# Kernel tuning notes

Hardware: AMD Instinct MI355X
Metric: run time of the kernel (lower is better)

## Reference

```python
import jax, jax.numpy as jnp
import numpy as np

LATENT = 128
N_NODES = 50000
N_EDGES = 800000
LN_EPS = 1e-5


def _glorot(key, fan_in, fan_out):
    lim = np.sqrt(6.0 / (fan_in + fan_out)).astype(np.float32)
    return jax.random.uniform(key, (fan_in, fan_out), jnp.float32, -lim, lim)


def setup_inputs() -> dict:
    key = jax.random.key(0)
    ks = jax.random.split(key, 10)
    node_latents = jax.random.normal(ks[0], (1, N_NODES, LATENT), jnp.float32)
    mesh_edge_latents = jax.random.normal(ks[1], (1, N_EDGES, LATENT), jnp.float32)
    senders = jax.random.randint(ks[2], (N_EDGES,), 0, N_NODES, jnp.int32)
    receivers = jax.random.randint(ks[3], (N_EDGES,), 0, N_NODES, jnp.int32)
    # mesh_edge_net: Linear(3L, L), ReLU, Linear(L, L), ReLU, LayerNorm(L)
    me_w1 = _glorot(ks[4], 3 * LATENT, LATENT)
    me_b1 = jnp.zeros((LATENT,), jnp.float32)
    me_w2 = _glorot(ks[5], LATENT, LATENT)
    me_b2 = jnp.zeros((LATENT,), jnp.float32)
    me_g = jnp.ones((LATENT,), jnp.float32)
    me_beta = jnp.zeros((LATENT,), jnp.float32)
    # node_feature_net: Linear(2L, L), ReLU, Linear(L, L), ReLU, LayerNorm(L)
    nf_w1 = _glorot(ks[6], 2 * LATENT, LATENT)
    nf_b1 = jnp.zeros((LATENT,), jnp.float32)
    nf_w2 = _glorot(ks[7], LATENT, LATENT)
    nf_b2 = jnp.zeros((LATENT,), jnp.float32)
    nf_g = jnp.ones((LATENT,), jnp.float32)
    nf_beta = jnp.zeros((LATENT,), jnp.float32)
    return dict(node_latents=node_latents, mesh_edge_latents=mesh_edge_latents,
                senders=senders, receivers=receivers,
                me_w1=me_w1, me_b1=me_b1, me_w2=me_w2, me_b2=me_b2, me_g=me_g, me_beta=me_beta,
                nf_w1=nf_w1, nf_b1=nf_b1, nf_w2=nf_w2, nf_b2=nf_b2, nf_g=nf_g, nf_beta=nf_beta)


def _mlp_ln(x, w1, b1, w2, b2, g, beta):
    h = jax.nn.relu(x @ w1 + b1)
    h = jax.nn.relu(h @ w2 + b2)
    mu = jnp.mean(h, axis=-1, keepdims=True)
    var = jnp.var(h, axis=-1, keepdims=True)
    return (h - mu) * jax.lax.rsqrt(var + LN_EPS) * g + beta


def reference(node_latents, mesh_edge_latents, senders, receivers,
              me_w1, me_b1, me_w2, me_b2, me_g, me_beta,
              nf_w1, nf_b1, nf_w2, nf_b2, nf_g, nf_beta):
    # gather sender/receiver node features: [B, E, L]
    edge_in = jnp.concatenate([node_latents[:, senders, :],
                               node_latents[:, receivers, :],
                               mesh_edge_latents], axis=-1)
    new_edges = _mlp_ln(edge_in, me_w1, me_b1, me_w2, me_b2, me_g, me_beta)
    # scatter_add messages to receiver nodes along dim=1
    aggr = jax.vmap(lambda e: jax.ops.segment_sum(e, receivers, num_segments=N_NODES))(new_edges)
    node_in = jnp.concatenate([node_latents, aggr], axis=-1)
    new_nodes = _mlp_ln(node_in, nf_w1, nf_b1, nf_w2, nf_b2, nf_g, nf_beta)
    new_nodes = new_nodes + node_latents  # residual
    new_edges = new_edges + mesh_edge_latents  # residual
    return new_nodes, new_edges
```

## Files before the change

kernel.cpp:

```cpp
#include <hip/hip_runtime.h>
#include <stdint.h>

typedef unsigned short u16;
typedef __bf16 bf16x8 __attribute__((ext_vector_type(8)));
typedef float f32x4 __attribute__((ext_vector_type(4)));

#define N_NODES 50000
#define N_EDGES 800000
#define LN_EPS 1e-5f

__device__ __forceinline__ uint4 pack8(const float* __restrict__ p) {
    const float4 f0 = ((const float4*)p)[0];
    const float4 f1 = ((const float4*)p)[1];
    union { __bf16 b[8]; uint4 q; } t;
    t.b[0] = (__bf16)f0.x; t.b[1] = (__bf16)f0.y; t.b[2] = (__bf16)f0.z; t.b[3] = (__bf16)f0.w;
    t.b[4] = (__bf16)f1.x; t.b[5] = (__bf16)f1.y; t.b[6] = (__bf16)f1.z; t.b[7] = (__bf16)f1.w;
    return t.q;
}

__global__ void pack_weights(const float* __restrict__ w1e, const float* __restrict__ w2e,
                             const float* __restrict__ w1n, const float* __restrict__ w2n,
                             uint4* __restrict__ out)
{
    const int t = blockIdx.x * 256 + threadIdx.x;
    const float* W; int idx;
    if (t < 6144)       { W = w1e; idx = t; }
    else if (t < 8192)  { W = w2e; idx = t - 6144; }
    else if (t < 12288) { W = w1n; idx = t - 8192; }
    else                { W = w2n; idx = t - 12288; }
    const int lane = idx & 63;
    const int col16 = (idx >> 6) & 7;
    const int kb = idx >> 9;
    const int row0 = kb * 32 + (lane >> 4) * 8;
    const int col = col16 * 16 + (lane & 15);
    union { __bf16 b[8]; uint4 q; } v;
#pragma unroll
    for (int j = 0; j < 8; ++j) v.b[j] = (__bf16)W[(size_t)(row0 + j) * 128 + col];
    out[t] = v.q;
}

__global__ void hist_kernel(const int* __restrict__ receivers, int* __restrict__ cnt) {
    const int e = blockIdx.x * 256 + threadIdx.x;
    if (e < N_EDGES) atomicAdd(&cnt[receivers[e]], 1);
}

__global__ void scan_kernel(const int* __restrict__ cnt, int* __restrict__ cursor) {
    __shared__ int sums[1024];
    const int t = threadIdx.x;
    const int CH = 49;
    const int base = t * CH;
    int s = 0;
#pragma unroll 1
    for (int i = 0; i < CH; ++i) { const int idx = base + i; if (idx < N_NODES) s += cnt[idx]; }
    sums[t] = s;
    __syncthreads();
    for (int off = 1; off < 1024; off <<= 1) {
        const int v = (t >= off) ? sums[t - off] : 0;
        __syncthreads();
        sums[t] += v;
        __syncthreads();
    }
    int run = sums[t] - s;
#pragma unroll 1
    for (int i = 0; i < CH; ++i) {
        const int idx = base + i;
        if (idx < N_NODES) { cursor[idx] = run; run += cnt[idx]; }
    }
}

__global__ void scatter_kernel(const int* __restrict__ receivers, int* __restrict__ cursor,
                               int* __restrict__ sorted_eid) {
    const int e = blockIdx.x * 256 + threadIdx.x;
    if (e < N_EDGES) {
        const int pos = atomicAdd(&cursor[receivers[e]], 1);
        sorted_eid[pos] = e;
    }
}

template<int SORTED>
__global__ __launch_bounds__(256, 3)
void edge_mlp_kernel(const float* __restrict__ node, const float* __restrict__ elat,
                     const int* __restrict__ senders, const int* __restrict__ receivers,
                     const int* __restrict__ sorted_eid,
                     const float* __restrict__ b1, const float* __restrict__ b2,
                     const float* __restrict__ gam, const float* __restrict__ bet,
                     const uint4* __restrict__ w1p, const uint4* __restrict__ w2p,
                     float* __restrict__ eout, float* __restrict__ aggr)
{
    __shared__ __align__(16) u16 x_lds[3 * 64 * 128];
    __shared__ int rcv_s[64];
    __shared__ int eid_s[64];
    __shared__ float2 part[256];
    __shared__ float muv[64], rsv[64];

    float* lnf = (float*)x_lds;

    const int tid = threadIdx.x;
    const int w = tid >> 6;
    const int lane = tid & 63;
    const int cl = lane & 15;
    const int q = lane >> 4;
    const int n_base = w * 32;

    float b1v[2], b2v[2], gv[2], bv[2];
#pragma unroll
    for (int n = 0; n < 2; ++n) {
        const int c = n_base + n * 16 + cl;
        b1v[n] = b1[c]; b2v[n] = b2[c];
        gv[n]  = gam[c]; bv[n] = bet[c];
    }

    for (int tile = blockIdx.x; tile < N_EDGES / 64; tile += gridDim.x) {
        const int base = tile * 64;

        {
            const int ch = tid & 15;
            const int r0 = tid >> 4;
#pragma unroll
            for (int gp = 0; gp < 4; ++gp) {
                const int row = gp * 16 + r0;
                const int rx = row & 7;
                const int eid = SORTED ? sorted_eid[base + row] : (base + row);
                const int sn = senders[eid];
                const int rc = receivers[eid];
                if (ch == 0) { rcv_s[row] = rc; eid_s[row] = eid; }
                uint4* dst = (uint4*)x_lds + row * 16;
                dst[ch ^ rx]          = pack8(node + (size_t)sn * 128 + ch * 8);
                dst[1024 + (ch ^ rx)] = pack8(node + (size_t)rc * 128 + ch * 8);
                dst[2048 + (ch ^ rx)] = pack8(elat + (size_t)eid * 128 + ch * 8);
            }
        }
        __syncthreads();

        f32x4 acc[4][2];
#pragma unroll
        for (int m = 0; m < 4; ++m)
#pragma unroll
            for (int n = 0; n < 2; ++n)
#pragma unroll
                for (int r = 0; r < 4; ++r) acc[m][n][r] = 0.f;

        uint4 wreg[14][2];
#pragma unroll
        for (int kb = 0; kb < 2; ++kb)
#pragma unroll
            for (int n = 0; n < 2; ++n)
                wreg[kb][n] = w1p[(kb * 8 + w * 2 + n) * 64 + lane];

#pragma unroll
        for (int kb = 0; kb < 12; ++kb) {
            if (kb + 2 < 12) {
#pragma unroll
                for (int n = 0; n < 2; ++n)
                    wreg[kb + 2][n] = w1p[((kb + 2) * 8 + w * 2 + n) * 64 + lane];
            }
            const int p = kb >> 2, k2 = kb & 3;
            bf16x8 a[4];
#pragma unroll
            for (int m = 0; m < 4; ++m) {
                const int row = m * 16 + cl;
                a[m] = __builtin_bit_cast(bf16x8,
                    ((const uint4*)x_lds)[p * 1024 + row * 16 + ((k2 * 4 + q) ^ (row & 7))]);
            }
#pragma unroll
            for (int m = 0; m < 4; ++m)
#pragma unroll
                for (int n = 0; n < 2; ++n)
                    acc[m][n] = __builtin_amdgcn_mfma_f32_16x16x32_bf16(
                        a[m], __builtin_bit_cast(bf16x8, wreg[kb][n]), acc[m][n], 0, 0, 0);
        }

        uint4 w2reg[4][2];
#pragma unroll
        for (int kb = 0; kb < 4; ++kb)
#pragma unroll
            for (int n = 0; n < 2; ++n)
                w2reg[kb][n] = w2p[(kb * 8 + w * 2 + n) * 64 + lane];

        __syncthreads();

        {
            __bf16* hb = (__bf16*)x_lds;
#pragma unroll
            for (int m = 0; m < 4; ++m)
#pragma unroll
                for (int n = 0; n < 2; ++n)
#pragma unroll
                    for (int r = 0; r < 4; ++r) {
                        const int row = m * 16 + q * 4 + r;
                        const int col = n_base + n * 16 + cl;
                        hb[row * 128 + (((col >> 3) ^ (row & 7)) << 3) + (col & 7)] =
                            (__bf16)fmaxf(acc[m][n][r] + b1v[n], 0.f);
                    }
        }
        __syncthreads();

#pragma unroll
        for (int m = 0; m < 4; ++m)
#pragma unroll
            for (int n = 0; n < 2; ++n)
#pragma unroll
                for (int r = 0; r < 4; ++r) acc[m][n][r] = 0.f;
#pragma unroll
        for (int kb = 0; kb < 4; ++kb) {
            bf16x8 a[4];
#pragma unroll
            for (int m = 0; m < 4; ++m) {
                const int row = m * 16 + cl;
                a[m] = __builtin_bit_cast(bf16x8,
                    ((const uint4*)x_lds)[row * 16 + ((kb * 4 + q) ^ (row & 7))]);
            }
#pragma unroll
            for (int m = 0; m < 4; ++m)
#pragma unroll
                for (int n = 0; n < 2; ++n)
                    acc[m][n] = __builtin_amdgcn_mfma_f32_16x16x32_bf16(
                        a[m], __builtin_bit_cast(bf16x8, w2reg[kb][n]), acc[m][n], 0, 0, 0);
        }

#pragma unroll
        for (int m = 0; m < 4; ++m)
#pragma unroll
            for (int n = 0; n < 2; ++n)
#pragma unroll
                for (int r = 0; r < 4; ++r)
                    acc[m][n][r] = fmaxf(acc[m][n][r] + b2v[n], 0.f);

#pragma unroll
        for (int m = 0; m < 4; ++m)
#pragma unroll
            for (int r = 0; r < 4; ++r) {
                float s  = acc[m][0][r] + acc[m][1][r];
                float ss = acc[m][0][r] * acc[m][0][r] + acc[m][1][r] * acc[m][1][r];
#pragma unroll
                for (int off = 1; off < 16; off <<= 1) {
                    s  += __shfl_xor(s, off, 64);
                    ss += __shfl_xor(ss, off, 64);
                }
                if (cl == 0) part[w * 64 + m * 16 + q * 4 + r] = make_float2(s, ss);
            }
        __syncthreads();
        if (tid < 64) {
            float s = 0.f, ss = 0.f;
#pragma unroll
            for (int ww = 0; ww < 4; ++ww) { const float2 pp = part[ww * 64 + tid]; s += pp.x; ss += pp.y; }
            const float mu = s * (1.f / 128.f);
            const float var = ss * (1.f / 128.f) - mu * mu;
            muv[tid] = mu;
            rsv[tid] = rsqrtf(var + LN_EPS);
        }
        __syncthreads();

#pragma unroll
        for (int m = 0; m < 4; ++m)
#pragma unroll
            for (int r = 0; r < 4; ++r) {
                const int row = m * 16 + q * 4 + r;
                const float mu = muv[row];
                const float rs = rsv[row];
                float* orow = eout + (size_t)eid_s[row] * 128;
#pragma unroll
                for (int n = 0; n < 2; ++n) {
                    const int col = n_base + n * 16 + cl;
                    const float ln = (acc[m][n][r] - mu) * rs * gv[n] + bv[n];
                    lnf[row * 128 + col] = ln;
                    const float e = (float)((__bf16*)x_lds)[16384 + row * 128 + (((col >> 3) ^ (row & 7)) << 3) + (col & 7)];
                    orow[col] = ln + e;
                }
            }
        __syncthreads();

        {
            const int c = tid & 127;
            const int h = tid >> 7;
            const int rstart = h * 32, rend = rstart + 32;
            float sacc = 0.f; int flushed = 0;
#pragma unroll 1
            for (int r = rstart; r < rend; ++r) {
                sacc += lnf[r * 128 + c];
                const int rc = rcv_s[r];
                const bool last = (r == 63);
                const bool bnd = last || (rc != rcv_s[r + 1]);
                if (bnd) {
                    float* dst = &aggr[(size_t)rc * 128 + c];
                    if (SORTED && !last && flushed) *dst = sacc;
                    else atomicAdd(dst, sacc);
                    sacc = 0.f; flushed = 1;
                }
            }
            if (sacc != 0.f)
                atomicAdd(&aggr[(size_t)rcv_s[rend - 1] * 128 + c], sacc);
        }
        __syncthreads();
    }
}

__global__ __launch_bounds__(256, 4)
void node_mlp_kernel(const float* __restrict__ node, const float* __restrict__ aggr,
                     const float* __restrict__ b1, const float* __restrict__ b2,
                     const float* __restrict__ gam, const float* __restrict__ bet,
                     const uint4* __restrict__ w1p, const uint4* __restrict__ w2p,
                     float* __restrict__ nout)
{
    __shared__ __align__(16) u16 x_lds[2 * 64 * 128];
    __shared__ float2 part[256];
    __shared__ float muv[64], rsv[64];

    const int tid = threadIdx.x;
    const int w = tid >> 6;
    const int lane = tid & 63;
    const int cl = lane & 15;
    const int q = lane >> 4;
    const int n_base = w * 32;

    float b1v[2], b2v[2], gv[2], bv[2];
#pragma unroll
    for (int n = 0; n < 2; ++n) {
        const int c = n_base + n * 16 + cl;
        b1v[n] = b1[c]; b2v[n] = b2[c];
        gv[n]  = gam[c]; bv[n] = bet[c];
    }

    const int ntiles = (N_NODES + 63) / 64;
    for (int tile = blockIdx.x; tile < ntiles; tile += gridDim.x) {
        const int base = tile * 64;

        {
            const int ch = tid & 15;
            const int r0 = tid >> 4;
#pragma unroll
            for (int gp = 0; gp < 4; ++gp) {
                const int row = gp * 16 + r0;
                const int rx = row & 7;
                int gn = base + row;
                if (gn >= N_NODES) gn = N_NODES - 1;
                uint4* dst = (uint4*)x_lds + row * 16;
                dst[ch ^ rx]          = pack8(node + (size_t)gn * 128 + ch * 8);
                dst[1024 + (ch ^ rx)] = pack8(aggr + (size_t)gn * 128 + ch * 8);
            }
        }
        __syncthreads();

        f32x4 acc[4][2];
#pragma unroll
        for (int m = 0; m < 4; ++m)
#pragma unroll
            for (int n = 0; n < 2; ++n)
#pragma unroll
                for (int r = 0; r < 4; ++r) acc[m][n][r] = 0.f;

        uint4 wreg[10][2];
#pragma unroll
        for (int kb = 0; kb < 2; ++kb)
#pragma unroll
            for (int n = 0; n < 2; ++n)
                wreg[kb][n] = w1p[(kb * 8 + w * 2 + n) * 64 + lane];

#pragma unroll
        for (int kb = 0; kb < 8; ++kb) {
            if (kb + 2 < 8) {
#pragma unroll
                for (int n = 0; n < 2; ++n)
                    wreg[kb + 2][n] = w1p[((kb + 2) * 8 + w * 2 + n) * 64 + lane];
            }
            const int p = kb >> 2, k2 = kb & 3;
            bf16x8 a[4];
#pragma unroll
            for (int m = 0; m < 4; ++m) {
                const int row = m * 16 + cl;
                a[m] = __builtin_bit_cast(bf16x8,
                    ((const uint4*)x_lds)[p * 1024 + row * 16 + ((k2 * 4 + q) ^ (row & 7))]);
            }
#pragma unroll
            for (int m = 0; m < 4; ++m)
#pragma unroll
                for (int n = 0; n < 2; ++n)
                    acc[m][n] = __builtin_amdgcn_mfma_f32_16x16x32_bf16(
                        a[m], __builtin_bit_cast(bf16x8, wreg[kb][n]), acc[m][n], 0, 0, 0);
        }

        uint4 w2reg[4][2];
#pragma unroll
        for (int kb = 0; kb < 4; ++kb)
#pragma unroll
            for (int n = 0; n < 2; ++n)
                w2reg[kb][n] = w2p[(kb * 8 + w * 2 + n) * 64 + lane];

        __syncthreads();

        {
            __bf16* hb = (__bf16*)(x_lds + 8192);
#pragma unroll
            for (int m = 0; m < 4; ++m)
#pragma unroll
                for (int n = 0; n < 2; ++n)
#pragma unroll
                    for (int r = 0; r < 4; ++r) {
                        const int row = m * 16 + q * 4 + r;
                        const int col = n_base + n * 16 + cl;
                        hb[row * 128 + (((col >> 3) ^ (row & 7)) << 3) + (col & 7)] =
                            (__bf16)fmaxf(acc[m][n][r] + b1v[n], 0.f);
                    }
        }
        __syncthreads();

#pragma unroll
        for (int m = 0; m < 4; ++m)
#pragma unroll
            for (int n = 0; n < 2; ++n)
#pragma unroll
                for (int r = 0; r < 4; ++r) acc[m][n][r] = 0.f;
#pragma unroll
        for (int kb = 0; kb < 4; ++kb) {
            bf16x8 a[4];
#pragma unroll
            for (int m = 0; m < 4; ++m) {
                const int row = m * 16 + cl;
                a[m] = __builtin_bit_cast(bf16x8,
                    ((const uint4*)x_lds)[1024 + row * 16 + ((kb * 4 + q) ^ (row & 7))]);
            }
#pragma unroll
            for (int m = 0; m < 4; ++m)
#pragma unroll
                for (int n = 0; n < 2; ++n)
                    acc[m][n] = __builtin_amdgcn_mfma_f32_16x16x32_bf16(
                        a[m], __builtin_bit_cast(bf16x8, w2reg[kb][n]), acc[m][n], 0, 0, 0);
        }
#pragma unroll
        for (int m = 0; m < 4; ++m)
#pragma unroll
            for (int n = 0; n < 2; ++n)
#pragma unroll
                for (int r = 0; r < 4; ++r)
                    acc[m][n][r] = fmaxf(acc[m][n][r] + b2v[n], 0.f);

#pragma unroll
        for (int m = 0; m < 4; ++m)
#pragma unroll
            for (int r = 0; r < 4; ++r) {
                float s  = acc[m][0][r] + acc[m][1][r];
                float ss = acc[m][0][r] * acc[m][0][r] + acc[m][1][r] * acc[m][1][r];
#pragma unroll
                for (int off = 1; off < 16; off <<= 1) {
                    s  += __shfl_xor(s, off, 64);
                    ss += __shfl_xor(ss, off, 64);
                }
                if (cl == 0) part[w * 64 + m * 16 + q * 4 + r] = make_float2(s, ss);
            }
        __syncthreads();
        if (tid < 64) {
            float s = 0.f, ss = 0.f;
#pragma unroll
            for (int ww = 0; ww < 4; ++ww) { const float2 pp = part[ww * 64 + tid]; s += pp.x; ss += pp.y; }
            const float mu = s * (1.f / 128.f);
            const float var = ss * (1.f / 128.f) - mu * mu;
            muv[tid] = mu;
            rsv[tid] = rsqrtf(var + LN_EPS);
        }
        __syncthreads();

#pragma unroll
        for (int m = 0; m < 4; ++m)
#pragma unroll
            for (int r = 0; r < 4; ++r) {
                const int row = m * 16 + q * 4 + r;
                if (base + row < N_NODES) {
                    const float mu = muv[row];
                    const float rs = rsv[row];
                    float* orow = nout + (size_t)(base + row) * 128;
#pragma unroll
                    for (int n = 0; n < 2; ++n) {
                        const int col = n_base + n * 16 + cl;
                        const float ln = (acc[m][n][r] - mu) * rs * gv[n] + bv[n];
                        const float e = (float)((__bf16*)x_lds)[row * 128 + (((col >> 3) ^ (row & 7)) << 3) + (col & 7)];
                        orow[col] = ln + e;
                    }
                }
            }
        __syncthreads();
    }
}

extern "C" void kernel_launch(void* const* d_in, const int* in_sizes, int n_in,
                              void* d_out, int out_size, void* d_ws, size_t ws_size,
                              hipStream_t stream) {
    (void)in_sizes; (void)n_in; (void)out_size;
    const float* node = (const float*)d_in[0];
    const float* elat = (const float*)d_in[1];
    const int* senders = (const int*)d_in[2];
    const int* receivers = (const int*)d_in[3];
    const float* me_w1 = (const float*)d_in[4];
    const float* me_b1 = (const float*)d_in[5];
    const float* me_w2 = (const float*)d_in[6];
    const float* me_b2 = (const float*)d_in[7];
    const float* me_g  = (const float*)d_in[8];
    const float* me_be = (const float*)d_in[9];
    const float* nf_w1 = (const float*)d_in[10];
    const float* nf_b1 = (const float*)d_in[11];
    const float* nf_w2 = (const float*)d_in[12];
    const float* nf_b2 = (const float*)d_in[13];
    const float* nf_g  = (const float*)d_in[14];
    const float* nf_be = (const float*)d_in[15];

    float* out_nodes = (float*)d_out;
    float* out_edges = out_nodes + (size_t)N_NODES * 128;

    char* ws = (char*)d_ws;
    const size_t off_aggr   = 0;
    const size_t off_wpack  = off_aggr  + (size_t)N_NODES * 128 * sizeof(float);
    const size_t off_cnt    = off_wpack + 14336 * sizeof(uint4);
    const size_t off_cursor = off_cnt   + (size_t)N_NODES * sizeof(int);
    const size_t off_sorted = off_cursor+ (size_t)N_NODES * sizeof(int);
    const size_t need_full  = off_sorted+ (size_t)N_EDGES * sizeof(int);
    const size_t need_min   = off_cnt;
    if (ws_size < need_min) return;

    float* aggr   = (float*)(ws + off_aggr);
    uint4* wpack  = (uint4*)(ws + off_wpack);
    int*   cnt    = (int*)(ws + off_cnt);
    int*   cursor = (int*)(ws + off_cursor);
    int*   sorted = (int*)(ws + off_sorted);
    const bool use_sort = (ws_size >= need_full);

    hipMemsetAsync(aggr, 0, (size_t)N_NODES * 128 * sizeof(float), stream);
    pack_weights<<<56, 256, 0, stream>>>(me_w1, me_w2, nf_w1, nf_w2, wpack);

    if (use_sort) {
        hipMemsetAsync(cnt, 0, (size_t)N_NODES * sizeof(int), stream);
        hist_kernel<<<(N_EDGES + 255) / 256, 256, 0, stream>>>(receivers, cnt);
        scan_kernel<<<1, 1024, 0, stream>>>(cnt, cursor);
        scatter_kernel<<<(N_EDGES + 255) / 256, 256, 0, stream>>>(receivers, cursor, sorted);
        edge_mlp_kernel<1><<<768, 256, 0, stream>>>(node, elat, senders, receivers, sorted,
                                                    me_b1, me_b2, me_g, me_be,
                                                    wpack, wpack + 6144,
                                                    out_edges, aggr);
    } else {
        edge_mlp_kernel<0><<<768, 256, 0, stream>>>(node, elat, senders, receivers, nullptr,
                                                    me_b1, me_b2, me_g, me_be,
                                                    wpack, wpack + 6144,
                                                    out_edges, aggr);
    }
    node_mlp_kernel<<<782, 256, 0, stream>>>(node, aggr,
                                             nf_b1, nf_b2, nf_g, nf_be,
                                             wpack + 8192, wpack + 12288,
                                             out_nodes);
}
```

Measured before the change: 1.162 ms.

## Pre-convert nodes to bf16, pre-permute edge latents, parallelize scan, chunk tiles

Node latents are converted to bf16 once, and edge latents are permuted into receiver-sorted bf16 order before the edge MLP. The gathers then copy bf16 rows directly instead of converting fp32 on every load. The single-block scan is replaced by a three-kernel parallel scan. The scatter also emits sorted sender and receiver arrays so the edge kernel avoids indirect index lookups, and each block now processes a contiguous, XCD-interleaved range of tiles. The trade-off is an extra full pass over the edge latents in permute_elat, plus reuse of the output buffer as scratch.

```diff
diff --git a/kernel.cpp b/kernel.cpp
--- a/kernel.cpp
+++ b/kernel.cpp
@@ -7,6 +7,7 @@
 
 #define N_NODES 50000
 #define N_EDGES 800000
+#define NTILES  (N_EDGES / 64)
 #define LN_EPS 1e-5f
 
 __device__ __forceinline__ uint4 pack8(const float* __restrict__ p) {
@@ -39,49 +40,82 @@
     out[t] = v.q;
 }
 
+__global__ void convert_node(const float* __restrict__ node, uint4* __restrict__ node_bf) {
+    const int idx = blockIdx.x * 256 + threadIdx.x;
+    node_bf[idx] = pack8(node + (size_t)(idx >> 4) * 128 + (idx & 15) * 8);
+}
+
 __global__ void hist_kernel(const int* __restrict__ receivers, int* __restrict__ cnt) {
     const int e = blockIdx.x * 256 + threadIdx.x;
     if (e < N_EDGES) atomicAdd(&cnt[receivers[e]], 1);
 }
 
-__global__ void scan_kernel(const int* __restrict__ cnt, int* __restrict__ cursor) {
-    __shared__ int sums[1024];
+#define SCAN_NB 196
+__global__ void scan1(const int* __restrict__ cnt, int* __restrict__ bsum) {
+    __shared__ int wsum[4];
+    const int i = blockIdx.x * 256 + threadIdx.x;
+    int v = (i < N_NODES) ? cnt[i] : 0;
+#pragma unroll
+    for (int off = 1; off < 64; off <<= 1) v += __shfl_xor(v, off, 64);
+    if ((threadIdx.x & 63) == 0) wsum[threadIdx.x >> 6] = v;
+    __syncthreads();
+    if (threadIdx.x == 0) bsum[blockIdx.x] = wsum[0] + wsum[1] + wsum[2] + wsum[3];
+}
+__global__ void scan2(const int* __restrict__ bsum, int* __restrict__ boff) {
+    __shared__ int s[256];
     const int t = threadIdx.x;
-    const int CH = 49;
-    const int base = t * CH;
-    int s = 0;
-#pragma unroll 1
-    for (int i = 0; i < CH; ++i) { const int idx = base + i; if (idx < N_NODES) s += cnt[idx]; }
-    sums[t] = s;
-    __syncthreads();
-    for (int off = 1; off < 1024; off <<= 1) {
-        const int v = (t >= off) ? sums[t - off] : 0;
-        __syncthreads();
-        sums[t] += v;
-        __syncthreads();
-    }
-    int run = sums[t] - s;
-#pragma unroll 1
-    for (int i = 0; i < CH; ++i) {
-        const int idx = base + i;
-        if (idx < N_NODES) { cursor[idx] = run; run += cnt[idx]; }
-    }
-}
-
-__global__ void scatter_kernel(const int* __restrict__ receivers, int* __restrict__ cursor,
-                               int* __restrict__ sorted_eid) {
+    const int v = (t < SCAN_NB) ? bsum[t] : 0;
+    s[t] = v; __syncthreads();
+    for (int off = 1; off < 256; off <<= 1) {
+        const int u = (t >= off) ? s[t - off] : 0;
+        __syncthreads(); s[t] += u; __syncthreads();
+    }
+    if (t < SCAN_NB) boff[t] = s[t] - v;
+}
+__global__ void scan3(const int* __restrict__ cnt, const int* __restrict__ boff,
+                      int* __restrict__ cursor) {
+    __shared__ int s[256];
+    const int i = blockIdx.x * 256 + threadIdx.x;
+    const int t = threadIdx.x;
+    const int v = (i < N_NODES) ? cnt[i] : 0;
+    s[t] = v; __syncthreads();
+    for (int off = 1; off < 256; off <<= 1) {
+        const int u = (t >= off) ? s[t - off] : 0;
+        __syncthreads(); s[t] += u; __syncthreads();
+    }
+    if (i < N_NODES) cursor[i] = boff[blockIdx.x] + s[t] - v;
+}
+
+__global__ void scatter_kernel(const int* __restrict__ senders, const int* __restrict__ receivers,
+                               int* __restrict__ cursor,
+                               int* __restrict__ sorted_eid, int* __restrict__ pos_of,
+                               int* __restrict__ snd_sorted, int* __restrict__ rcv_sorted) {
     const int e = blockIdx.x * 256 + threadIdx.x;
     if (e < N_EDGES) {
-        const int pos = atomicAdd(&cursor[receivers[e]], 1);
+        const int rc = receivers[e];
+        const int pos = atomicAdd(&cursor[rc], 1);
         sorted_eid[pos] = e;
-    }
+        pos_of[e] = pos;
+        snd_sorted[pos] = senders[e];
+        rcv_sorted[pos] = rc;
+    }
+}
+
+__global__ void permute_elat(const float* __restrict__ elat, const int* __restrict__ pos_of,
+                             uint4* __restrict__ elat_s) {
+    const int idx = blockIdx.x * 256 + threadIdx.x;
+    const int e = idx >> 4, ch = idx & 15;
+    const int p = pos_of[e];
+    elat_s[(size_t)p * 16 + ch] = pack8(elat + (size_t)e * 128 + ch * 8);
 }
 
 template<int SORTED>
 __global__ __launch_bounds__(256, 3)
-void edge_mlp_kernel(const float* __restrict__ node, const float* __restrict__ elat,
+void edge_mlp_kernel(const u16* __restrict__ node_bf, const float* __restrict__ elat,
+                     const u16* __restrict__ elat_s,
                      const int* __restrict__ senders, const int* __restrict__ receivers,
                      const int* __restrict__ sorted_eid,
+                     const int* __restrict__ snd_sorted, const int* __restrict__ rcv_sorted,
                      const float* __restrict__ b1, const float* __restrict__ b2,
                      const float* __restrict__ gam, const float* __restrict__ bet,
                      const uint4* __restrict__ w1p, const uint4* __restrict__ w2p,
@@ -110,7 +144,12 @@
         gv[n]  = gam[c]; bv[n] = bet[c];
     }
 
-    for (int tile = blockIdx.x; tile < N_EDGES / 64; tile += gridDim.x) {
+    const int nchunk = gridDim.x;
+    const int chunk = (blockIdx.x & 7) * (nchunk >> 3) + (blockIdx.x >> 3);
+    const int t_lo = (int)(((long long)chunk * NTILES) / nchunk);
+    const int t_hi = (int)(((long long)(chunk + 1) * NTILES) / nchunk);
+
+    for (int tile = t_lo; tile < t_hi; ++tile) {
         const int base = tile * 64;
 
         {
@@ -120,14 +159,21 @@
             for (int gp = 0; gp < 4; ++gp) {
                 const int row = gp * 16 + r0;
                 const int rx = row & 7;
-                const int eid = SORTED ? sorted_eid[base + row] : (base + row);
-                const int sn = senders[eid];
-                const int rc = receivers[eid];
+                const int p = base + row;
+                int sn, rc, eid;
+                if (SORTED) {
+                    sn = snd_sorted[p]; rc = rcv_sorted[p]; eid = sorted_eid[p];
+                } else {
+                    sn = senders[p]; rc = receivers[p]; eid = p;
+                }
                 if (ch == 0) { rcv_s[row] = rc; eid_s[row] = eid; }
                 uint4* dst = (uint4*)x_lds + row * 16;
-                dst[ch ^ rx]          = pack8(node + (size_t)sn * 128 + ch * 8);
-                dst[1024 + (ch ^ rx)] = pack8(node + (size_t)rc * 128 + ch * 8);
-                dst[2048 + (ch ^ rx)] = pack8(elat + (size_t)eid * 128 + ch * 8);
+                dst[ch ^ rx]          = ((const uint4*)(node_bf + (size_t)sn * 128))[ch];
+                dst[1024 + (ch ^ rx)] = ((const uint4*)(node_bf + (size_t)rc * 128))[ch];
+                if (SORTED)
+                    dst[2048 + (ch ^ rx)] = ((const uint4*)(elat_s + (size_t)p * 128))[ch];
+                else
+                    dst[2048 + (ch ^ rx)] = pack8(elat + (size_t)p * 128 + ch * 8);
             }
         }
         __syncthreads();
@@ -505,37 +551,56 @@
     float* out_nodes = (float*)d_out;
     float* out_edges = out_nodes + (size_t)N_NODES * 128;
 
+    char* ob = (char*)d_out;
+    u16* node_bf    = (u16*)ob;
+    int* sorted_eid = (int*)(ob + 12800000);
+    int* pos_of     = (int*)(ob + 16000000);
+    int* snd_sorted = (int*)(ob + 19200000);
+    int* rcv_sorted = (int*)(ob + 22400000);
+
     char* ws = (char*)d_ws;
     const size_t off_aggr   = 0;
     const size_t off_wpack  = off_aggr  + (size_t)N_NODES * 128 * sizeof(float);
     const size_t off_cnt    = off_wpack + 14336 * sizeof(uint4);
     const size_t off_cursor = off_cnt   + (size_t)N_NODES * sizeof(int);
-    const size_t off_sorted = off_cursor+ (size_t)N_NODES * sizeof(int);
-    const size_t need_full  = off_sorted+ (size_t)N_EDGES * sizeof(int);
-    const size_t need_min   = off_cnt;
-    if (ws_size < need_min) return;
+    const size_t off_scan   = off_cursor+ (size_t)N_NODES * sizeof(int);
+    const size_t off_elat_s = off_scan  + 4096;
+    const size_t need_b     = off_cnt;
+    const size_t need_a     = off_elat_s + (size_t)N_EDGES * 128 * sizeof(u16);
+    if (ws_size < need_b) return;
 
     float* aggr   = (float*)(ws + off_aggr);
     uint4* wpack  = (uint4*)(ws + off_wpack);
     int*   cnt    = (int*)(ws + off_cnt);
     int*   cursor = (int*)(ws + off_cursor);
-    int*   sorted = (int*)(ws + off_sorted);
-    const bool use_sort = (ws_size >= need_full);
+    int*   bsum   = (int*)(ws + off_scan);
+    int*   boff   = (int*)(ws + off_scan + 2048);
+    u16*   elat_s = (u16*)(ws + off_elat_s);
+    const bool tier_a = (ws_size >= need_a);
 
     hipMemsetAsync(aggr, 0, (size_t)N_NODES * 128 * sizeof(float), stream);
     pack_weights<<<56, 256, 0, stream>>>(me_w1, me_w2, nf_w1, nf_w2, wpack);
-
-    if (use_sort) {
+    convert_node<<<3125, 256, 0, stream>>>(node, (uint4*)node_bf);
+
+    if (tier_a) {
         hipMemsetAsync(cnt, 0, (size_t)N_NODES * sizeof(int), stream);
         hist_kernel<<<(N_EDGES + 255) / 256, 256, 0, stream>>>(receivers, cnt);
-        scan_kernel<<<1, 1024, 0, stream>>>(cnt, cursor);
-        scatter_kernel<<<(N_EDGES + 255) / 256, 256, 0, stream>>>(receivers, cursor, sorted);
-        edge_mlp_kernel<1><<<768, 256, 0, stream>>>(node, elat, senders, receivers, sorted,
+        scan1<<<SCAN_NB, 256, 0, stream>>>(cnt, bsum);
+        scan2<<<1, 256, 0, stream>>>(bsum, boff);
+        scan3<<<SCAN_NB, 256, 0, stream>>>(cnt, boff, cursor);
+        scatter_kernel<<<(N_EDGES + 255) / 256, 256, 0, stream>>>(
+            senders, receivers, cursor, sorted_eid, pos_of, snd_sorted, rcv_sorted);
+        permute_elat<<<50000, 256, 0, stream>>>(elat, pos_of, (uint4*)elat_s);
+        edge_mlp_kernel<1><<<768, 256, 0, stream>>>(node_bf, elat, elat_s,
+                                                    senders, receivers,
+                                                    sorted_eid, snd_sorted, rcv_sorted,
                                                     me_b1, me_b2, me_g, me_be,
                                                     wpack, wpack + 6144,
                                                     out_edges, aggr);
     } else {
-        edge_mlp_kernel<0><<<768, 256, 0, stream>>>(node, elat, senders, receivers, nullptr,
+        edge_mlp_kernel<0><<<768, 256, 0, stream>>>(node_bf, elat, elat_s,
+                                                    senders, receivers,
+                                                    sorted_eid, snd_sorted, rcv_sorted,
                                                     me_b1, me_b2, me_g, me_be,
                                                     wpack, wpack + 6144,
                                                     out_edges, aggr);
```

New measurement: 1.117 ms. -3.9%, faster.
